# Kernel tuning notes

Measured on AMD Instinct MI355X. Metric: run time of the kernel, lower is better.

Reference implementation:

```python
import jax, jax.numpy as jnp
import numpy as np

N, E = 50000, 400000          # nodes, edges (avg degree 8)
DIN, DEIN = 128, 128          # in_node_feats, in_edge_feats
H, DE, DN = 8, 16, 16         # num_heads, out_edge_feats, out_node_feats
HDE = H * DE                  # 128


def setup_inputs() -> dict:
    key = jax.random.key(0)
    ks = jax.random.split(key, 14)
    nfeats = jax.random.normal(ks[0], (N, DIN), jnp.float32)
    efeats = jax.random.normal(ks[1], (E, DEIN), jnp.float32)
    norm = jax.random.uniform(ks[2], (E, 1), jnp.float32)
    src = jax.random.randint(ks[3], (E,), 0, N, jnp.int32)
    # guarantee every node has in-degree >= 1 (module raises on 0-in-degree)
    dst = jnp.concatenate([jax.random.permutation(ks[4], N).astype(jnp.int32),
                           jax.random.randint(ks[5], (E - N,), 0, N, jnp.int32)])
    s = 0.05
    W_ni = jax.random.normal(ks[6], (HDE, DIN), jnp.float32) * s
    W_nj = jax.random.normal(ks[7], (HDE, DIN), jnp.float32) * s
    W_fij = jax.random.normal(ks[8], (HDE, DEIN), jnp.float32) * s
    W_edges = jax.random.normal(ks[9], (HDE, 3 * HDE), jnp.float32) * s
    W_attn = jax.random.normal(ks[10], (H, DE), jnp.float32) * s
    bias = jnp.zeros((HDE,), jnp.float32)
    W_node = jax.random.normal(ks[11], (H * DN, DIN), jnp.float32) * s
    b_node = jnp.zeros((H * DN,), jnp.float32)
    return dict(nfeats=nfeats, efeats=efeats, norm=norm, src=src, dst=dst,
                W_ni=W_ni, W_nj=W_nj, W_fij=W_fij, W_edges=W_edges,
                W_attn=W_attn, bias=bias, W_node=W_node, b_node=b_node)


def reference(nfeats, efeats, norm, src, dst,
              W_ni, W_nj, W_fij, W_edges, W_attn, bias, W_node, b_node):
    # node/edge linear projections
    f_ni = nfeats @ W_ni.T            # [N, H*De]
    f_nj = nfeats @ W_nj.T            # [N, H*De]
    f_eij = efeats @ W_fij.T          # [E, H*De]
    # fc_edges(cat[f_ni[src], f_eij, f_nj[dst]]) == sum of 3 block-matmuls;
    # project on nodes/edges FIRST, then gather (same math, less edge traffic)
    W1, W2, W3 = jnp.split(W_edges, 3, axis=1)   # each [H*De, H*De]
    t_src = f_ni @ W1.T               # [N, H*De]
    t_e = f_eij @ W2.T                # [E, H*De]
    t_dst = f_nj @ W3.T               # [N, H*De]
    f_lin = t_src[src] + t_e + t_dst[dst]         # [E, H*De]
    f = jax.nn.leaky_relu(f_lin)                  # slope 0.01 == torch default
    f_out = (f + bias).reshape(E, H, DE)          # [E, H, De]
    # fc_attn then sum over head-out dim == dot with column-sum of W_attn
    a = jnp.einsum('ehd,d->eh', f_out, W_attn.sum(0))   # [E, H]
    # edge_softmax over edges incoming to each dst node, per head
    m = jax.ops.segment_max(a, dst, num_segments=N)     # [N, H]
    ex = jnp.exp(a - m[dst])
    den = jax.ops.segment_sum(ex, dst, num_segments=N)  # [N, H]
    alpha = (ex / den[dst])[:, :, None]                 # [E, H, 1]
    # mpnn_type='node': message = h_out[src] * a * norm, reduced by sum at dst
    h_node = (nfeats @ W_node.T + b_node).reshape(N, H, DN)
    msg = h_node[src] * alpha * norm[:, :, None]        # [E, H, Dn]
    h_out = jax.ops.segment_sum(msg, dst, num_segments=N)  # [N, H, Dn]
    return h_out.sum(axis=1), f_out.sum(axis=1)
```

## Files before the change

kernel.cpp:

```cpp
#include <hip/hip_runtime.h>

typedef unsigned short ushort_t;
typedef __attribute__((ext_vector_type(8))) short short8;
typedef __attribute__((ext_vector_type(4))) float f32x4;
typedef __attribute__((ext_vector_type(4))) int i32x4;

#define NN 50000
#define NE 400000
#define WS_NEED 46531200ull

static __device__ __forceinline__ float bf2f(ushort_t u) {
    union { unsigned int i; float f; } v; v.i = ((unsigned int)u) << 16; return v.f;
}
static __device__ __forceinline__ ushort_t f2bf(float f) {
    unsigned int u = __float_as_uint(f);
    u = (u + 0x7fffu + ((u >> 16) & 1u)) >> 16;
    return (ushort_t)u;
}
static __device__ __forceinline__ float loadf(const void* base, size_t i, int f32) {
    return f32 ? ((const float*)base)[i] : bf2f(((const ushort_t*)base)[i]);
}
static __device__ __forceinline__ short8 load8(const void* base, size_t off, int f32) {
    if (f32) {
        const float* p = (const float*)base + off;
        const f32x4 a = *(const f32x4*)p;
        const f32x4 b = *(const f32x4*)(p + 4);
        short8 r;
#pragma unroll
        for (int i = 0; i < 4; i++) { r[i] = (short)f2bf(a[i]); r[i + 4] = (short)f2bf(b[i]); }
        return r;
    }
    return *(const short8*)((const ushort_t*)base + off);
}

__global__ void k_detect(const ushort_t* __restrict__ nf, int* __restrict__ flag) {
    if (threadIdx.x == 0) {
        int cnt = 0;
        for (int i = 0; i < 512; i += 2) {
            const int eb = (nf[i] >> 7) & 0xFF;
            cnt += (eb >= 0xB0);
        }
        *flag = (cnt > 8) ? 1 : 0;
    }
}

__global__ void k_zero(float* __restrict__ p, int n) {
    const int i = blockIdx.x * 256 + threadIdx.x;
    if (i < n) p[i] = 0.f;
}

__global__ void k_recip(float* __restrict__ p, int n) {
    const int i = blockIdx.x * 256 + threadIdx.x;
    if (i < n) p[i] = 1.f / fmaxf(p[i], 1e-30f);
}

__global__ void k_prep(const void* __restrict__ W_ni, const void* __restrict__ W_nj,
                       const void* __restrict__ W_fij, const void* __restrict__ W_edges,
                       const void* __restrict__ W_attn, const void* __restrict__ W_node,
                       const int* __restrict__ flag,
                       ushort_t* __restrict__ Wcat, ushort_t* __restrict__ Ae,
                       float* __restrict__ wsum) {
    const int f32 = *flag;
    int r = blockIdx.x;
    int k = threadIdx.x;
    if (r == 0 && k < 16) {
        float s = 0.f;
        for (int h = 0; h < 8; h++) s += loadf(W_attn, h * 16 + k, f32);
        wsum[k] = s;
    }
    float acc = 0.f;
    if (r < 128) {
        for (int m = 0; m < 128; m++)
            acc += loadf(W_edges, r * 384 + m, f32) * loadf(W_ni, m * 128 + k, f32);
        Wcat[r * 128 + k] = f2bf(acc);
    } else if (r < 256) {
        int j = r - 128;
        for (int m = 0; m < 128; m++)
            acc += loadf(W_edges, j * 384 + 256 + m, f32) * loadf(W_nj, m * 128 + k, f32);
        Wcat[r * 128 + k] = f2bf(acc);
    } else if (r < 384) {
        Wcat[r * 128 + k] = f2bf(loadf(W_node, (r - 256) * 128 + k, f32));
    } else {
        int j = r - 384;
        for (int m = 0; m < 128; m++)
            acc += loadf(W_edges, j * 384 + 128 + m, f32) * loadf(W_fij, m * 128 + k, f32);
        Ae[j * 128 + (k ^ ((j & 7) << 3))] = f2bf(acc);
    }
}

__global__ __launch_bounds__(256) void k_nodes(const void* __restrict__ X,
                                               const ushort_t* __restrict__ Wcat,
                                               const void* __restrict__ b_node,
                                               const int* __restrict__ flag,
                                               ushort_t* __restrict__ tsrc,
                                               ushort_t* __restrict__ tdst,
                                               ushort_t* __restrict__ hnode) {
    const int f32 = *flag;
    const int lane = threadIdx.x & 63, wave = threadIdx.x >> 6;
    const int c = lane & 15, quad = lane >> 4;
    const int m0 = blockIdx.x * 64 + wave * 16;

    f32x4 acc[24];
#pragma unroll
    for (int t = 0; t < 24; t++) acc[t] = (f32x4){0.f, 0.f, 0.f, 0.f};

    int arow = m0 + c;
    if (arow >= NN) arow = NN - 1;

#pragma unroll
    for (int k4 = 0; k4 < 4; k4++) {
        const int kb = k4 * 32 + quad * 8;
        short8 a = load8(X, (size_t)arow * 128 + kb, f32);
#pragma unroll
        for (int t = 0; t < 24; t++) {
            short8 b = *(const short8*)(Wcat + (size_t)(t * 16 + c) * 128 + kb);
            acc[t] = __builtin_amdgcn_mfma_f32_16x16x32_bf16(a, b, acc[t], 0, 0, 0);
        }
    }

    float bnv[8];
#pragma unroll
    for (int t = 0; t < 8; t++) bnv[t] = loadf(b_node, t * 16 + c, f32);

#pragma unroll
    for (int g = 0; g < 3; g++) {
        ushort_t* dp = (g == 0) ? tsrc : (g == 1) ? tdst : hnode;
#pragma unroll
        for (int r = 0; r < 4; r++) {
            const int m = m0 + quad * 4 + r;
            short8 v;
#pragma unroll
            for (int t = 0; t < 8; t++) {
                const float badd = (g == 2) ? bnv[t] : 0.f;
                v[t] = (short)f2bf(acc[g * 8 + t][r] + badd);
            }
            if (m < NN) *(short8*)(dp + (size_t)m * 128 + c * 8) = v;
        }
    }
}

__global__ __launch_bounds__(256) void k_edges(const void* __restrict__ EF,
                                               const ushort_t* __restrict__ Ae,
                                               const int* __restrict__ src,
                                               const int* __restrict__ dst,
                                               const ushort_t* __restrict__ tsrc,
                                               const ushort_t* __restrict__ tdst,
                                               const void* __restrict__ bias,
                                               const float* __restrict__ wsum,
                                               const int* __restrict__ flag,
                                               ushort_t* __restrict__ exw,
                                               float* __restrict__ den,
                                               float* __restrict__ out1) {
    __shared__ ushort_t sAe[128 * 128];
    const int f32 = *flag;
    const int lane = threadIdx.x & 63, wave = threadIdx.x >> 6;
    const int c = lane & 15, quad = lane >> 4;
    const int e0 = (blockIdx.x * 4 + wave) * 16;

#pragma unroll
    for (int it = 0; it < 8; it++) {
        const int idx = (it * 256 + threadIdx.x) * 8;
        *(short8*)(sAe + idx) = *(const short8*)(Ae + idx);
    }
    __syncthreads();

    const int ebase = e0 + quad * 4;
    const i32x4 sv4 = *(const i32x4*)(src + ebase);
    const i32x4 dv4 = *(const i32x4*)(dst + ebase);

    f32x4 acc[8];
#pragma unroll
    for (int t = 0; t < 8; t++) acc[t] = (f32x4){0.f, 0.f, 0.f, 0.f};

    const int arow = e0 + c;
#pragma unroll
    for (int k4 = 0; k4 < 4; k4++) {
        const int kb = k4 * 32 + quad * 8;
        short8 a = load8(EF, (size_t)arow * 128 + kb, f32);
#pragma unroll
        for (int t = 0; t < 8; t++) {
            short8 b = *(const short8*)(sAe + (size_t)(t * 16 + c) * 128 + (kb ^ ((c & 7) << 3)));
            acc[t] = __builtin_amdgcn_mfma_f32_16x16x32_bf16(a, b, acc[t], 0, 0, 0);
        }
    }

    short8 ts8[4], td8[4];
#pragma unroll
    for (int r = 0; r < 4; r++) {
        ts8[r] = *(const short8*)(tsrc + (size_t)sv4[r] * 128 + c * 8);
        td8[r] = *(const short8*)(tdst + (size_t)dv4[r] * 128 + c * 8);
    }

    const float wc = wsum[c];
    float biasv[8];
#pragma unroll
    for (int t = 0; t < 8; t++) biasv[t] = loadf(bias, t * 16 + c, f32);

#pragma unroll
    for (int r = 0; r < 4; r++) {
        const int e = ebase + r;
        const int dv = dv4[r];
        float o1 = 0.f, part[8];
#pragma unroll
        for (int t = 0; t < 8; t++) {
            float f = acc[t][r] + bf2f((ushort_t)ts8[r][t]) + bf2f((ushort_t)td8[r][t]);
            f = (f > 0.f) ? f : 0.01f * f;
            const float fo = f + biasv[t];
            o1 += fo;
            part[t] = fo * wc;
        }
        out1[(size_t)e * 16 + c] = o1;
#pragma unroll
        for (int t = 0; t < 8; t++) {
            part[t] += __shfl_xor(part[t], 1);
            part[t] += __shfl_xor(part[t], 2);
            part[t] += __shfl_xor(part[t], 4);
            part[t] += __shfl_xor(part[t], 8);
        }
        if (c < 8) {
            float av = part[0];
#pragma unroll
            for (int t = 1; t < 8; t++)
                if (c == t) av = part[t];
            av = fminf(fmaxf(av, -50.f), 50.f);
            const float ex = __expf(av);
            const ushort_t exb16 = f2bf(ex);
            exw[(size_t)e * 8 + c] = exb16;
            atomicAdd(&den[(size_t)dv * 8 + c], bf2f(exb16));
        }
    }
}

__global__ __launch_bounds__(256) void k_msg(const int* __restrict__ src,
                                             const int* __restrict__ dst,
                                             const void* __restrict__ norm,
                                             const ushort_t* __restrict__ hnode,
                                             const ushort_t* __restrict__ exw,
                                             const float* __restrict__ den,
                                             const int* __restrict__ flag,
                                             float* __restrict__ out0) {
    const int f32 = *flag;
    const int tid = blockIdx.x * 256 + threadIdx.x;
    const int e = tid >> 4, d = tid & 15;
    if (e >= NE) return;
    const int sv = src[e], dv = dst[e];
    const float nm = loadf(norm, e, f32);
    const short8 hn = *(const short8*)(hnode + (size_t)sv * 128 + d * 8);
    const short8 ew = *(const short8*)(exw + (size_t)e * 8);
    const f32x4* rd = (const f32x4*)(den + (size_t)dv * 8);
    const f32x4 r0 = rd[0], r1 = rd[1];
    float s = 0.f;
#pragma unroll
    for (int h = 0; h < 4; h++)
        s += bf2f((ushort_t)hn[h]) * (bf2f((ushort_t)ew[h]) * r0[h]);
#pragma unroll
    for (int h = 0; h < 4; h++)
        s += bf2f((ushort_t)hn[4 + h]) * (bf2f((ushort_t)ew[4 + h]) * r1[h]);
    atomicAdd(&out0[(size_t)dv * 16 + d], s * nm);
}

extern "C" void kernel_launch(void* const* d_in, const int* in_sizes, int n_in,
                              void* d_out, int out_size, void* d_ws, size_t ws_size,
                              hipStream_t stream) {
    const void* nfeats  = d_in[0];
    const void* efeats  = d_in[1];
    const void* norm    = d_in[2];
    const int*  src     = (const int*)d_in[3];
    const int*  dst     = (const int*)d_in[4];
    const void* W_ni    = d_in[5];
    const void* W_nj    = d_in[6];
    const void* W_fij   = d_in[7];
    const void* W_edges = d_in[8];
    const void* W_attn  = d_in[9];
    const void* bias    = d_in[10];
    const void* W_node  = d_in[11];
    const void* b_node  = d_in[12];

    if (ws_size < WS_NEED) {
        k_zero<<<(out_size + 255) / 256, 256, 0, stream>>>((float*)d_out, out_size);
        return;
    }

    char* ws = (char*)d_ws;
    const size_t o_den   = 0;
    const size_t o_exw   = 1600000;
    const size_t o_wcat  = 8000000;
    const size_t o_ae    = 8098304;
    const size_t o_wsum  = 8131072;
    const size_t o_flag  = 8131136;
    const size_t o_tsrc  = 8131200;
    const size_t o_tdst  = o_tsrc + 12800000;
    const size_t o_hnode = o_tdst + 12800000;

    float*    den   = (float*)(ws + o_den);
    ushort_t* exw   = (ushort_t*)(ws + o_exw);
    ushort_t* Wcat  = (ushort_t*)(ws + o_wcat);
    ushort_t* Ae    = (ushort_t*)(ws + o_ae);
    float*    wsum  = (float*)(ws + o_wsum);
    int*      flag  = (int*)(ws + o_flag);
    ushort_t* tsrc  = (ushort_t*)(ws + o_tsrc);
    ushort_t* tdst  = (ushort_t*)(ws + o_tdst);
    ushort_t* hnode = (ushort_t*)(ws + o_hnode);

    float* out0 = (float*)d_out;
    float* out1 = (float*)d_out + NN * 16;

    k_detect<<<1, 64, 0, stream>>>((const ushort_t*)nfeats, flag);
    k_zero<<<(NN * 8 + 255) / 256, 256, 0, stream>>>(den, NN * 8);
    k_zero<<<(NN * 16 + 255) / 256, 256, 0, stream>>>(out0, NN * 16);
    k_prep<<<512, 128, 0, stream>>>(W_ni, W_nj, W_fij, W_edges, W_attn, W_node, flag, Wcat, Ae, wsum);
    k_nodes<<<(NN + 63) / 64, 256, 0, stream>>>(nfeats, Wcat, b_node, flag, tsrc, tdst, hnode);
    k_edges<<<NE / 64, 256, 0, stream>>>(efeats, Ae, src, dst, tsrc, tdst, bias, wsum, flag, exw, den, out1);
    k_recip<<<(NN * 8 + 255) / 256, 256, 0, stream>>>(den, NN * 8);
    k_msg<<<NE * 16 / 256, 256, 0, stream>>>(src, dst, norm, hnode, exw, den, flag, out0);
}
```

Baseline: 465.1 us.

## Persistent-style edge and node GEMM kernels with LDS weights and prefetch

k_nodes now splits the three output projections across blocks. Each block stages one 128x128 swizzled weight slice in LDS and loops over three row tiles, instead of reading all 24 weight tiles from global memory. k_edges is templated on input precision, processes five 64-edge chunks per block, and software-prefetches the next chunk's edge features and indices while computing the current one. The per-head attention reduction is replaced by a butterfly transpose-reduce that uses fewer shuffles. The cost is fewer blocks (786 and 1250) and higher register pressure in the prefetch loop.

```diff
diff --git a/kernel.cpp b/kernel.cpp
--- a/kernel.cpp
+++ b/kernel.cpp
@@ -68,18 +68,19 @@
         for (int h = 0; h < 8; h++) s += loadf(W_attn, h * 16 + k, f32);
         wsum[k] = s;
     }
+    const int ks = k ^ ((r & 7) << 3);
     float acc = 0.f;
     if (r < 128) {
         for (int m = 0; m < 128; m++)
             acc += loadf(W_edges, r * 384 + m, f32) * loadf(W_ni, m * 128 + k, f32);
-        Wcat[r * 128 + k] = f2bf(acc);
+        Wcat[r * 128 + ks] = f2bf(acc);
     } else if (r < 256) {
         int j = r - 128;
         for (int m = 0; m < 128; m++)
             acc += loadf(W_edges, j * 384 + 256 + m, f32) * loadf(W_nj, m * 128 + k, f32);
-        Wcat[r * 128 + k] = f2bf(acc);
+        Wcat[r * 128 + ks] = f2bf(acc);
     } else if (r < 384) {
-        Wcat[r * 128 + k] = f2bf(loadf(W_node, (r - 256) * 128 + k, f32));
+        Wcat[r * 128 + ks] = f2bf(loadf(W_node, (r - 256) * 128 + k, f32));
     } else {
         int j = r - 384;
         for (int m = 0; m < 128; m++)
@@ -95,46 +96,191 @@
                                                ushort_t* __restrict__ tsrc,
                                                ushort_t* __restrict__ tdst,
                                                ushort_t* __restrict__ hnode) {
+    __shared__ ushort_t sW[128 * 128];
     const int f32 = *flag;
+    const int g = blockIdx.x % 3;
+    const int tch = blockIdx.x / 3;
     const int lane = threadIdx.x & 63, wave = threadIdx.x >> 6;
     const int c = lane & 15, quad = lane >> 4;
-    const int m0 = blockIdx.x * 64 + wave * 16;
-
-    f32x4 acc[24];
-#pragma unroll
-    for (int t = 0; t < 24; t++) acc[t] = (f32x4){0.f, 0.f, 0.f, 0.f};
-
-    int arow = m0 + c;
-    if (arow >= NN) arow = NN - 1;
-
-#pragma unroll
-    for (int k4 = 0; k4 < 4; k4++) {
-        const int kb = k4 * 32 + quad * 8;
-        short8 a = load8(X, (size_t)arow * 128 + kb, f32);
-#pragma unroll
-        for (int t = 0; t < 24; t++) {
-            short8 b = *(const short8*)(Wcat + (size_t)(t * 16 + c) * 128 + kb);
-            acc[t] = __builtin_amdgcn_mfma_f32_16x16x32_bf16(a, b, acc[t], 0, 0, 0);
-        }
-    }
-
+
+    const ushort_t* Wg = Wcat + (size_t)g * 16384;
+#pragma unroll
+    for (int it2 = 0; it2 < 8; it2++) {
+        const int idx = (it2 * 256 + threadIdx.x) * 8;
+        *(short8*)(sW + idx) = *(const short8*)(Wg + idx);
+    }
+    __syncthreads();
+
+    ushort_t* const outp = (g == 0) ? tsrc : (g == 1) ? tdst : hnode;
     float bnv[8];
 #pragma unroll
-    for (int t = 0; t < 8; t++) bnv[t] = loadf(b_node, t * 16 + c, f32);
-
-#pragma unroll
-    for (int g = 0; g < 3; g++) {
-        ushort_t* dp = (g == 0) ? tsrc : (g == 1) ? tdst : hnode;
+    for (int t = 0; t < 8; t++) bnv[t] = (g == 2) ? loadf(b_node, t * 16 + c, f32) : 0.f;
+
+    for (int it = 0; it < 3; it++) {
+        const int tile = tch * 3 + it;
+        if (tile * 64 >= NN) break;
+        const int m0 = tile * 64 + wave * 16;
+        int arow = m0 + c;
+        if (arow >= NN) arow = NN - 1;
+        short8 a[4];
+#pragma unroll
+        for (int k4 = 0; k4 < 4; k4++)
+            a[k4] = load8(X, (size_t)arow * 128 + k4 * 32 + quad * 8, f32);
+        f32x4 acc[8];
+#pragma unroll
+        for (int t = 0; t < 8; t++) acc[t] = (f32x4){0.f, 0.f, 0.f, 0.f};
+#pragma unroll
+        for (int k4 = 0; k4 < 4; k4++) {
+            const int ks = (k4 * 32 + quad * 8) ^ ((c & 7) << 3);
+#pragma unroll
+            for (int t = 0; t < 8; t++) {
+                short8 b = *(const short8*)(sW + (size_t)(t * 16 + c) * 128 + ks);
+                acc[t] = __builtin_amdgcn_mfma_f32_16x16x32_bf16(a[k4], b, acc[t], 0, 0, 0);
+            }
+        }
 #pragma unroll
         for (int r = 0; r < 4; r++) {
             const int m = m0 + quad * 4 + r;
             short8 v;
 #pragma unroll
+            for (int t = 0; t < 8; t++) v[t] = (short)f2bf(acc[t][r] + bnv[t]);
+            if (m < NN) *(short8*)(outp + (size_t)m * 128 + c * 8) = v;
+        }
+    }
+}
+
+template<int F32>
+static __device__ __forceinline__ void edges_body(
+    const void* __restrict__ EF, const ushort_t* sAe,
+    const int* __restrict__ src, const int* __restrict__ dst,
+    const ushort_t* __restrict__ tsrc, const ushort_t* __restrict__ tdst,
+    const void* __restrict__ bias, const float* __restrict__ wsum,
+    ushort_t* __restrict__ exw, float* __restrict__ den, float* __restrict__ out1) {
+    const int lane = threadIdx.x & 63, wave = threadIdx.x >> 6;
+    const int c = lane & 15, quad = lane >> 4;
+
+    const float wc = wsum[c];
+    float biasv[8];
+#pragma unroll
+    for (int t = 0; t < 8; t++) biasv[t] = loadf(bias, t * 16 + c, F32);
+
+    const int ew0 = blockIdx.x * 320 + wave * 16;
+    i32x4 svn = *(const i32x4*)(src + ew0 + quad * 4);
+    i32x4 dvn = *(const i32x4*)(dst + ew0 + quad * 4);
+    f32x4 raw[8];
+    short8 an[4];
+    {
+        const size_t base = (size_t)(ew0 + c) * 128 + quad * 8;
+        if (F32) {
+            const float* p = (const float*)EF;
+#pragma unroll
+            for (int k4 = 0; k4 < 4; k4++) {
+                raw[k4 * 2]     = *(const f32x4*)(p + base + k4 * 32);
+                raw[k4 * 2 + 1] = *(const f32x4*)(p + base + k4 * 32 + 4);
+            }
+        } else {
+            const ushort_t* p = (const ushort_t*)EF;
+#pragma unroll
+            for (int k4 = 0; k4 < 4; k4++) an[k4] = *(const short8*)(p + base + k4 * 32);
+        }
+    }
+
+    for (int it = 0; it < 5; it++) {
+        const int ecur = ew0 + it * 64;
+        const i32x4 sv4 = svn, dv4 = dvn;
+        short8 a[4];
+        if (F32) {
+#pragma unroll
+            for (int k4 = 0; k4 < 4; k4++) {
+#pragma unroll
+                for (int j = 0; j < 4; j++) {
+                    a[k4][j]     = (short)f2bf(raw[k4 * 2][j]);
+                    a[k4][j + 4] = (short)f2bf(raw[k4 * 2 + 1][j]);
+                }
+            }
+        } else {
+#pragma unroll
+            for (int k4 = 0; k4 < 4; k4++) a[k4] = an[k4];
+        }
+        short8 ts8[4], td8[4];
+#pragma unroll
+        for (int r = 0; r < 4; r++) {
+            ts8[r] = *(const short8*)(tsrc + (size_t)sv4[r] * 128 + c * 8);
+            td8[r] = *(const short8*)(tdst + (size_t)dv4[r] * 128 + c * 8);
+        }
+        if (it < 4) {
+            const int en = ecur + 64;
+            svn = *(const i32x4*)(src + en + quad * 4);
+            dvn = *(const i32x4*)(dst + en + quad * 4);
+            const size_t base = (size_t)(en + c) * 128 + quad * 8;
+            if (F32) {
+                const float* p = (const float*)EF;
+#pragma unroll
+                for (int k4 = 0; k4 < 4; k4++) {
+                    raw[k4 * 2]     = *(const f32x4*)(p + base + k4 * 32);
+                    raw[k4 * 2 + 1] = *(const f32x4*)(p + base + k4 * 32 + 4);
+                }
+            } else {
+                const ushort_t* p = (const ushort_t*)EF;
+#pragma unroll
+                for (int k4 = 0; k4 < 4; k4++) an[k4] = *(const short8*)(p + base + k4 * 32);
+            }
+        }
+        f32x4 acc[8];
+#pragma unroll
+        for (int t = 0; t < 8; t++) acc[t] = (f32x4){0.f, 0.f, 0.f, 0.f};
+#pragma unroll
+        for (int k4 = 0; k4 < 4; k4++) {
+            const int ks = (k4 * 32 + quad * 8) ^ ((c & 7) << 3);
+#pragma unroll
             for (int t = 0; t < 8; t++) {
-                const float badd = (g == 2) ? bnv[t] : 0.f;
-                v[t] = (short)f2bf(acc[g * 8 + t][r] + badd);
-            }
-            if (m < NN) *(short8*)(dp + (size_t)m * 128 + c * 8) = v;
+                short8 b = *(const short8*)(sAe + (size_t)(t * 16 + c) * 128 + ks);
+                acc[t] = __builtin_amdgcn_mfma_f32_16x16x32_bf16(a[k4], b, acc[t], 0, 0, 0);
+            }
+        }
+#pragma unroll
+        for (int r = 0; r < 4; r++) {
+            const int e = ecur + quad * 4 + r;
+            const int dv = dv4[r];
+            float o1 = 0.f, part[8];
+#pragma unroll
+            for (int t = 0; t < 8; t++) {
+                float f = acc[t][r] + bf2f((ushort_t)ts8[r][t]) + bf2f((ushort_t)td8[r][t]);
+                f = (f > 0.f) ? f : 0.01f * f;
+                const float fo = f + biasv[t];
+                o1 += fo;
+                part[t] = fo * wc;
+            }
+            out1[(size_t)e * 16 + c] = o1;
+            float q[4];
+#pragma unroll
+            for (int i2 = 0; i2 < 4; i2++) {
+                const float send  = (c & 8) ? part[i2] : part[i2 + 4];
+                const float other = __shfl_xor(send, 8);
+                const float mine  = (c & 8) ? part[i2 + 4] : part[i2];
+                q[i2] = mine + other;
+            }
+            float p2[2];
+#pragma unroll
+            for (int i2 = 0; i2 < 2; i2++) {
+                const float send  = (c & 4) ? q[i2] : q[i2 + 2];
+                const float other = __shfl_xor(send, 4);
+                const float mine  = (c & 4) ? q[i2 + 2] : q[i2];
+                p2[i2] = mine + other;
+            }
+            const float send  = (c & 2) ? p2[0] : p2[1];
+            const float other = __shfl_xor(send, 2);
+            const float mine  = (c & 2) ? p2[1] : p2[0];
+            float p1 = mine + other;
+            p1 += __shfl_xor(p1, 1);
+            if (!(c & 1)) {
+                const int h = c >> 1;
+                const float av = fminf(fmaxf(p1, -50.f), 50.f);
+                const float ex = __expf(av);
+                const ushort_t exb16 = f2bf(ex);
+                exw[(size_t)e * 8 + h] = exb16;
+                atomicAdd(&den[(size_t)dv * 8 + h], bf2f(exb16));
+            }
         }
     }
 }
@@ -152,83 +298,14 @@
                                                float* __restrict__ den,
                                                float* __restrict__ out1) {
     __shared__ ushort_t sAe[128 * 128];
-    const int f32 = *flag;
-    const int lane = threadIdx.x & 63, wave = threadIdx.x >> 6;
-    const int c = lane & 15, quad = lane >> 4;
-    const int e0 = (blockIdx.x * 4 + wave) * 16;
-
-#pragma unroll
-    for (int it = 0; it < 8; it++) {
-        const int idx = (it * 256 + threadIdx.x) * 8;
+#pragma unroll
+    for (int it2 = 0; it2 < 8; it2++) {
+        const int idx = (it2 * 256 + threadIdx.x) * 8;
         *(short8*)(sAe + idx) = *(const short8*)(Ae + idx);
     }
     __syncthreads();
-
-    const int ebase = e0 + quad * 4;
-    const i32x4 sv4 = *(const i32x4*)(src + ebase);
-    const i32x4 dv4 = *(const i32x4*)(dst + ebase);
-
-    f32x4 acc[8];
-#pragma unroll
-    for (int t = 0; t < 8; t++) acc[t] = (f32x4){0.f, 0.f, 0.f, 0.f};
-
-    const int arow = e0 + c;
-#pragma unroll
-    for (int k4 = 0; k4 < 4; k4++) {
-        const int kb = k4 * 32 + quad * 8;
-        short8 a = load8(EF, (size_t)arow * 128 + kb, f32);
-#pragma unroll
-        for (int t = 0; t < 8; t++) {
-            short8 b = *(const short8*)(sAe + (size_t)(t * 16 + c) * 128 + (kb ^ ((c & 7) << 3)));
-            acc[t] = __builtin_amdgcn_mfma_f32_16x16x32_bf16(a, b, acc[t], 0, 0, 0);
-        }
-    }
-
-    short8 ts8[4], td8[4];
-#pragma unroll
-    for (int r = 0; r < 4; r++) {
-        ts8[r] = *(const short8*)(tsrc + (size_t)sv4[r] * 128 + c * 8);
-        td8[r] = *(const short8*)(tdst + (size_t)dv4[r] * 128 + c * 8);
-    }
-
-    const float wc = wsum[c];
-    float biasv[8];
-#pragma unroll
-    for (int t = 0; t < 8; t++) biasv[t] = loadf(bias, t * 16 + c, f32);
-
-#pragma unroll
-    for (int r = 0; r < 4; r++) {
-        const int e = ebase + r;
-        const int dv = dv4[r];
-        float o1 = 0.f, part[8];
-#pragma unroll
-        for (int t = 0; t < 8; t++) {
-            float f = acc[t][r] + bf2f((ushort_t)ts8[r][t]) + bf2f((ushort_t)td8[r][t]);
-            f = (f > 0.f) ? f : 0.01f * f;
-            const float fo = f + biasv[t];
-            o1 += fo;
-            part[t] = fo * wc;
-        }
-        out1[(size_t)e * 16 + c] = o1;
-#pragma unroll
-        for (int t = 0; t < 8; t++) {
-            part[t] += __shfl_xor(part[t], 1);
-            part[t] += __shfl_xor(part[t], 2);
-            part[t] += __shfl_xor(part[t], 4);
-            part[t] += __shfl_xor(part[t], 8);
-        }
-        if (c < 8) {
-            float av = part[0];
-#pragma unroll
-            for (int t = 1; t < 8; t++)
-                if (c == t) av = part[t];
-            av = fminf(fmaxf(av, -50.f), 50.f);
-            const float ex = __expf(av);
-            const ushort_t exb16 = f2bf(ex);
-            exw[(size_t)e * 8 + c] = exb16;
-            atomicAdd(&den[(size_t)dv * 8 + c], bf2f(exb16));
-        }
-    }
+    if (*flag) edges_body<1>(EF, sAe, src, dst, tsrc, tdst, bias, wsum, exw, den, out1);
+    else       edges_body<0>(EF, sAe, src, dst, tsrc, tdst, bias, wsum, exw, den, out1);
 }
 
 __global__ __launch_bounds__(256) void k_msg(const int* __restrict__ src,
@@ -309,8 +386,8 @@
     k_zero<<<(NN * 8 + 255) / 256, 256, 0, stream>>>(den, NN * 8);
     k_zero<<<(NN * 16 + 255) / 256, 256, 0, stream>>>(out0, NN * 16);
     k_prep<<<512, 128, 0, stream>>>(W_ni, W_nj, W_fij, W_edges, W_attn, W_node, flag, Wcat, Ae, wsum);
-    k_nodes<<<(NN + 63) / 64, 256, 0, stream>>>(nfeats, Wcat, b_node, flag, tsrc, tdst, hnode);
-    k_edges<<<NE / 64, 256, 0, stream>>>(efeats, Ae, src, dst, tsrc, tdst, bias, wsum, flag, exw, den, out1);
+    k_nodes<<<786, 256, 0, stream>>>(nfeats, Wcat, b_node, flag, tsrc, tdst, hnode);
+    k_edges<<<1250, 256, 0, stream>>>(efeats, Ae, src, dst, tsrc, tdst, bias, wsum, flag, exw, den, out1);
     k_recip<<<(NN * 8 + 255) / 256, 256, 0, stream>>>(den, NN * 8);
     k_msg<<<NE * 16 / 256, 256, 0, stream>>>(src, dst, norm, hnode, exw, den, flag, out0);
 }
```

Result: faster. 443.2 us (-4.7%).
